# Kernel tuning notes

Hardware: AMD Instinct MI355X
Metric: run time of the kernel (lower is better)

The kernel has to match this reference:

```python
import jax, jax.numpy as jnp
import numpy as np

DN = ('NCHW', 'OIHW', 'NCHW')
A, NC = 3, 80  # num_anchors, num_classes


def conv(x, w, b, pad=1):
    y = jax.lax.conv_general_dilated(x, w, (1, 1), [(pad, pad), (pad, pad)], dimension_numbers=DN)
    return y + b[None, :, None, None]


def up2(x):
    return jnp.repeat(jnp.repeat(x, 2, axis=2), 2, axis=3)


def gen_anchors():
    # AnchorGenerator: sizes per level, 3 aspect ratios, 1 scale, stride=2**(i+3)
    sizes = [32.0, 64.0, 128.0]
    ars = [0.5, 1.0, 2.0]
    hw = [(64, 64), (32, 32), (16, 16)]
    out = []
    for i, ((h, w), bs) in enumerate(zip(hw, sizes)):
        stride = 2.0 ** (i + 3)
        base = np.array([[-bs * np.sqrt(a) / 2, -bs / np.sqrt(a) / 2,
                          bs * np.sqrt(a) / 2, bs / np.sqrt(a) / 2] for a in ars], dtype=np.float32)
        sx = np.arange(w, dtype=np.float32) * stride
        sy = np.arange(h, dtype=np.float32) * stride
        yy, xx = np.meshgrid(sy, sx, indexing='ij')  # torch.meshgrid default 'ij'
        shifts = np.stack([xx.ravel(), yy.ravel(), xx.ravel(), yy.ravel()], axis=1)
        anc = (base[None, :, :] + shifts[:, None, :]).reshape(-1, 4)
        out.append(anc)
    return jnp.asarray(np.concatenate(out, axis=0))


def setup_inputs() -> dict:
    key = jax.random.key(0)
    ks = jax.random.split(key, 32)
    def w(k, o, i, kh, kw):
        return jax.random.normal(k, (o, i, kh, kw), jnp.float32) * 0.02
    B = 8
    inp = {
        'feat3': jax.random.normal(ks[0], (B, 512, 64, 64), jnp.float32),
        'feat4': jax.random.normal(ks[1], (B, 1024, 32, 32), jnp.float32),
        'feat5': jax.random.normal(ks[2], (B, 2048, 16, 16), jnp.float32),
        # FPN lateral 1x1 convs
        'lw0': w(ks[3], 256, 512, 1, 1),  'lb0': jnp.zeros(256, jnp.float32),
        'lw1': w(ks[4], 256, 1024, 1, 1), 'lb1': jnp.zeros(256, jnp.float32),
        'lw2': w(ks[5], 256, 2048, 1, 1), 'lb2': jnp.zeros(256, jnp.float32),
        # FPN 3x3 output convs
        'fw0': w(ks[6], 256, 256, 3, 3), 'fb0': jnp.zeros(256, jnp.float32),
        'fw1': w(ks[7], 256, 256, 3, 3), 'fb1': jnp.zeros(256, jnp.float32),
        'fw2': w(ks[8], 256, 256, 3, 3), 'fb2': jnp.zeros(256, jnp.float32),
        # cls tower (shared across levels)
        'cw0': w(ks[9], 256, 256, 3, 3),  'cb0': jnp.zeros(256, jnp.float32),
        'cw1': w(ks[10], 256, 256, 3, 3), 'cb1': jnp.zeros(256, jnp.float32),
        'cw2': w(ks[11], A * NC, 256, 3, 3), 'cb2': jnp.zeros(A * NC, jnp.float32),
        # reg tower (shared across levels)
        'rw0': w(ks[12], 256, 256, 3, 3), 'rb0': jnp.zeros(256, jnp.float32),
        'rw1': w(ks[13], 256, 256, 3, 3), 'rb1': jnp.zeros(256, jnp.float32),
        'rw2': w(ks[14], A * 4, 256, 3, 3), 'rb2': jnp.zeros(A * 4, jnp.float32),
    }
    return inp


def _tower(f, w0, b0, w1, b1, w2, b2):
    x = jax.nn.relu(conv(f, w0, b0))
    x = jax.nn.relu(conv(x, w1, b1))
    return conv(x, w2, b2)


def reference(feat3, feat4, feat5,
              lw0, lb0, lw1, lb1, lw2, lb2,
              fw0, fb0, fw1, fb1, fw2, fb2,
              cw0, cb0, cw1, cb1, cw2, cb2,
              rw0, rb0, rw1, rb1, rw2, rb2):
    B = feat3.shape[0]
    # FPN: lateral 1x1 convs + top-down nearest upsample fusion + 3x3 convs
    l0 = conv(feat3, lw0, lb0, pad=0)
    l1 = conv(feat4, lw1, lb1, pad=0)
    l2 = conv(feat5, lw2, lb2, pad=0)
    l1 = l1 + up2(l2)
    l0 = l0 + up2(l1)
    feats = [conv(l0, fw0, fb0), conv(l1, fw1, fb1), conv(l2, fw2, fb2)]
    cls_list, reg_list = [], []
    for f in feats:
        c = _tower(f, cw0, cb0, cw1, cb1, cw2, cb2)  # [B, A*NC, H, W]
        r = _tower(f, rw0, rb0, rw1, rb1, rw2, rb2)  # [B, A*4, H, W]
        H, W = c.shape[2], c.shape[3]
        # view(B, A, C, HW).permute(0, 3, 1, 2) -> [B, HW, A, C]
        c = c.reshape(B, A, NC, H * W).transpose(0, 3, 1, 2)
        r = r.reshape(B, A, 4, H * W).transpose(0, 3, 1, 2)
        cls_list.append(c.reshape(B, H * W, A * NC))
        reg_list.append(r.reshape(B, H * W, A * 4))
    cls_all = jnp.concatenate(cls_list, axis=1)   # [B, 5376, 240]
    reg_all = jnp.concatenate(reg_list, axis=1)   # [B, 5376, 12]
    out = jnp.concatenate([cls_all, reg_all], axis=-1)  # [B, 5376, 252]
    anchors = gen_anchors()  # [16128, 4]
    return out, anchors
```

## Files before the change

kernel.cpp:

```cpp
#include <hip/hip_runtime.h>

typedef __bf16 bf16_t;
typedef __bf16 bf16x8 __attribute__((ext_vector_type(8)));
typedef float f32x4 __attribute__((ext_vector_type(4)));

__device__ inline void gl_lds16(const bf16_t* g, bf16_t* l) {
  __builtin_amdgcn_global_load_lds(
      (const __attribute__((address_space(1))) void*)g,
      (__attribute__((address_space(3))) void*)l, 16, 0, 0);
}

__global__ __launch_bounds__(256)
void nchw_to_nhwc(const float* __restrict__ in, bf16_t* __restrict__ out,
                  int C, int HW) {
  __shared__ float tile[64][65];
  const int n = blockIdx.z;
  const int c0 = blockIdx.y * 64, p0 = blockIdx.x * 64;
  const int t = threadIdx.x;
  const float* src = in + ((size_t)n * C + c0) * HW + p0;
  const int cl = t >> 6;
  const int pl = t & 63;
#pragma unroll
  for (int i = 0; i < 16; ++i)
    tile[cl + i * 4][pl] = src[(size_t)(cl + i * 4) * HW + pl];
  __syncthreads();
  bf16_t* dst = out + ((size_t)n * HW + p0) * C + c0;
  const int pc = t >> 6;
  const int cc = t & 63;
#pragma unroll
  for (int i = 0; i < 16; ++i)
    dst[(size_t)(pc + i * 4) * C + cc] = (bf16_t)tile[cc][pc + i * 4];
}

struct WSrc {
  const float *lw0, *lw1, *lw2;
  const float* w9[9];
  int O9[9];
};
__global__ __launch_bounds__(256)
void weight_prep(WSrc s, bf16_t* __restrict__ LWT0, bf16_t* __restrict__ LWT1,
                 bf16_t* __restrict__ LWT2, bf16_t* __restrict__ W33) {
  int idx = blockIdx.x * 256 + threadIdx.x;
  if (idx < 131072) { LWT0[idx] = (bf16_t)s.lw0[idx]; return; }
  if (idx < 393216) { int i = idx - 131072; LWT1[i] = (bf16_t)s.lw1[i]; return; }
  if (idx < 917504) { int i = idx - 393216; LWT2[i] = (bf16_t)s.lw2[i]; return; }
  int t2 = idx - 917504;
  if (t2 >= 9 * 589824) return;
  int sgi = t2 / 589824;
  int r = t2 - sgi * 589824;
  int kid = r >> 16;
  int rem = r & 65535;
  int o = rem >> 8, ci = rem & 255;
  const float* src = s.w9[sgi];
  int O = s.O9[sgi];
  W33[t2] = (o < O) ? (bf16_t)src[((size_t)o * 256 + ci) * 9 + kid] : (bf16_t)0.0f;
}

__global__ __launch_bounds__(256)
void up2_add_p(bf16_t* __restrict__ dst, const bf16_t* __restrict__ src,
               int lw, int lhw, int dWp, int dNs, int sWp, int sNs, int tot8) {
  int idx = blockIdx.x * 256 + threadIdx.x;
  if (idx >= tot8) return;
  const int c8 = idx & 31;
  const int pos = idx >> 5;
  const int n = pos >> lhw;
  const int rem = pos & ((1 << lhw) - 1);
  const int y = rem >> lw, x = rem & ((1 << lw) - 1);
  bf16_t* d = dst + ((size_t)n * dNs + (y + 1) * dWp + (x + 1)) * 256 + c8 * 8;
  const bf16_t* sp = src + ((size_t)n * sNs + ((y >> 1) + 1) * sWp + ((x >> 1) + 1)) * 256 + c8 * 8;
  bf16x8 dv = *(bf16x8*)d;
  bf16x8 sv = *(const bf16x8*)sp;
#pragma unroll
  for (int k = 0; k < 8; ++k) dv[k] = (bf16_t)((float)dv[k] + (float)sv[k]);
  *(bf16x8*)d = dv;
}

struct Job1 {
  const bf16_t* A;
  const bf16_t* Wt;
  const float* bias;
  bf16_t* outb;
  int mtiles, lw, lhw, oWp, onstride, Cin, pad0, pad1;
};
struct Job1Pack { Job1 j[3]; };

__global__ __launch_bounds__(256, 2)
void conv1_batch(Job1Pack jp) {
  __shared__ __align__(16) bf16_t As[128 * 32];
  __shared__ __align__(16) bf16_t Bs[128 * 32];
  int b = blockIdx.x, ji = 0;
#pragma unroll 1
  for (; ji < 2; ++ji) {
    int sz = jp.j[ji].mtiles * 2;
    if (b < sz) break;
    b -= sz;
  }
  const Job1 J = jp.j[ji];
  const int nt = b & 1, mt = b >> 1;
  const int m0 = mt * 128, n0 = nt * 128;
  const int t = threadIdx.x, l = t & 63, w = t >> 6;
  const int W = 1 << J.lw, HW = 1 << J.lhw;
  const int sr = l >> 2, seg = (l & 3) * 8;
  const bf16_t* aptr[2];
  const bf16_t* bptr[2];
  bf16_t* alds[2];
  bf16_t* blds[2];
#pragma unroll
  for (int q = 0; q < 2; ++q) {
    const int r = w * 32 + q * 16 + sr;
    aptr[q] = J.A + (size_t)(m0 + r) * J.Cin + seg;
    alds[q] = &As[(w * 32 + q * 16) * 32];
    bptr[q] = J.Wt + (size_t)(n0 + r) * J.Cin + seg;
    blds[q] = &Bs[(w * 32 + q * 16) * 32];
  }
  const int fr = l & 15, qd = l >> 4;
  const int wm = (w & 1) * 64, wn = (w >> 1) * 64;

  f32x4 acc[4][4];
#pragma unroll
  for (int i = 0; i < 4; ++i)
#pragma unroll
    for (int j = 0; j < 4; ++j)
#pragma unroll
      for (int r = 0; r < 4; ++r) acc[i][j][r] = 0.0f;

  const int kiters = J.Cin >> 5;
#pragma unroll 1
  for (int kk = 0; kk < kiters; ++kk) {
    __syncthreads();
    gl_lds16(aptr[0], alds[0]);
    gl_lds16(aptr[1], alds[1]);
    gl_lds16(bptr[0], blds[0]);
    gl_lds16(bptr[1], blds[1]);
    __syncthreads();
    aptr[0] += 32; aptr[1] += 32; bptr[0] += 32; bptr[1] += 32;
    bf16x8 af[4], bfv[4];
#pragma unroll
    for (int i = 0; i < 4; ++i)
      af[i] = *(const bf16x8*)&As[(wm + i * 16 + fr) * 32 + qd * 8];
#pragma unroll
    for (int j = 0; j < 4; ++j)
      bfv[j] = *(const bf16x8*)&Bs[(wn + j * 16 + fr) * 32 + qd * 8];
#pragma unroll
    for (int i = 0; i < 4; ++i)
#pragma unroll
      for (int j = 0; j < 4; ++j)
        acc[i][j] = __builtin_amdgcn_mfma_f32_16x16x32_bf16(af[i], bfv[j],
                                                            acc[i][j], 0, 0, 0);
  }

#pragma unroll
  for (int i = 0; i < 4; ++i) {
    const int mrow = m0 + wm + i * 16 + qd * 4;
#pragma unroll
    for (int j = 0; j < 4; ++j) {
      const int co = n0 + wn + j * 16 + fr;
      const float bv = J.bias[co];
#pragma unroll
      for (int r = 0; r < 4; ++r) {
        float v = acc[i][j][r] + bv;
        const int m = mrow + r;
        const int n = m >> J.lhw, hw = m & (HW - 1);
        const int y = hw >> J.lw, x = hw & (W - 1);
        J.outb[((size_t)n * J.onstride + (y + 1) * J.oWp + (x + 1)) * 256 + co] =
            (bf16_t)v;
      }
    }
  }
}

struct Job3 {
  const bf16_t* A;
  const bf16_t* Wt;
  const float* bias;
  bf16_t* outb;
  int mtiles, ntiles, lw, lhw, Wp, nsA, oWp, onstride;
  int relu, Cout, pos_off, ch_off, use_outf, nAr, Pc, pad_;
};
struct Job3Pack { Job3 j[6]; };

__global__ __launch_bounds__(256, 3)
void conv3_batch(Job3Pack jp, float* __restrict__ outf) {
  __shared__ __align__(16) bf16_t As[320 * 32];
  __shared__ __align__(16) bf16_t Bs[384 * 32];
  int b = blockIdx.x, ji = 0;
#pragma unroll 1
  for (; ji < 5; ++ji) {
    int sz = jp.j[ji].mtiles * jp.j[ji].ntiles;
    if (b < sz) break;
    b -= sz;
  }
  const Job3 J = jp.j[ji];
  const int nt = (J.ntiles == 2) ? (b & 1) : 0;
  const int mt = (J.ntiles == 2) ? (b >> 1) : b;
  const int m0 = mt * 128, n0 = nt * 128;
  const int t = threadIdx.x, l = t & 63, w = t >> 6;
  const int W = 1 << J.lw, HW = 1 << J.lhw;
  const int sr = l >> 2, seg = (l & 3) * 8;
  const int fr = l & 15, qd = l >> 4;
  const int wm = (w & 1) * 64, wn = (w >> 1) * 64;

  const int n_img = m0 >> J.lhw;
  const int Y0 = (m0 & (HW - 1)) >> J.lw;
  const bf16_t* Ag = J.A + ((size_t)n_img * J.nsA + (size_t)Y0 * J.Wp) * 256;

  int apix[4];
#pragma unroll
  for (int i = 0; i < 4; ++i) {
    const int m = wm + i * 16 + fr;
    const int y = m >> J.lw, x = m & (W - 1);
    apix[i] = ((y + 1) * J.Wp + (x + 1)) * 32 + qd * 8;
  }

  f32x4 acc[4][4];
#pragma unroll
  for (int i = 0; i < 4; ++i)
#pragma unroll
    for (int j = 0; j < 4; ++j)
#pragma unroll
      for (int r = 0; r < 4; ++r) acc[i][j][r] = 0.0f;

#pragma unroll 1
  for (int cb = 0; cb < 8; ++cb) {
    const int cboff = cb * 32;
#pragma unroll 1
    for (int ky = 0; ky < 3; ++ky) {
      __syncthreads();
#pragma unroll
      for (int r = 0; r < 6; ++r) {
        const int R = r * 64 + w * 16 + sr;
        const int tp = R >> 7, co = R & 127;
        gl_lds16(J.Wt + (size_t)(ky * 3 + tp) * 65536 +
                     (size_t)(n0 + co) * 256 + cboff + seg,
                 &Bs[(r * 64 + w * 16) * 32]);
      }
      if (ky == 0) {
#pragma unroll 1
        for (int r = 0; r < J.nAr; ++r) {
          int p = r * 64 + w * 16 + sr;
          p = (p < J.Pc) ? p : (J.Pc - 1);
          gl_lds16(Ag + (size_t)p * 256 + cboff + seg,
                   &As[(r * 64 + w * 16) * 32]);
        }
      }
      __syncthreads();
      const int dyoff = (ky - 1) * J.Wp * 32;
#pragma unroll
      for (int kx = 0; kx < 3; ++kx) {
        const int d = dyoff + (kx - 1) * 32;
        bf16x8 af[4], bfv[4];
#pragma unroll
        for (int i = 0; i < 4; ++i)
          af[i] = *(const bf16x8*)&As[apix[i] + d];
#pragma unroll
        for (int j = 0; j < 4; ++j)
          bfv[j] = *(const bf16x8*)&Bs[(kx * 128 + wn + j * 16 + fr) * 32 + qd * 8];
#pragma unroll
        for (int i = 0; i < 4; ++i)
#pragma unroll
          for (int j = 0; j < 4; ++j)
            acc[i][j] = __builtin_amdgcn_mfma_f32_16x16x32_bf16(af[i], bfv[j],
                                                                acc[i][j], 0, 0, 0);
      }
    }
  }

#pragma unroll
  for (int i = 0; i < 4; ++i) {
    const int mrow = m0 + wm + i * 16 + qd * 4;
#pragma unroll
    for (int j = 0; j < 4; ++j) {
      const int co = n0 + wn + j * 16 + fr;
      if (co < J.Cout) {
        const float bv = J.bias[co];
#pragma unroll
        for (int r = 0; r < 4; ++r) {
          float v = acc[i][j][r] + bv;
          if (J.relu) v = fmaxf(v, 0.0f);
          const int m = mrow + r;
          const int n = m >> J.lhw, hw = m & (HW - 1);
          if (J.use_outf) {
            outf[((size_t)n * 5376 + J.pos_off + hw) * 252 + J.ch_off + co] = v;
          } else {
            const int y = hw >> J.lw, x = hw & (W - 1);
            J.outb[((size_t)n * J.onstride + (y + 1) * J.oWp + (x + 1)) * 256 + co] =
                (bf16_t)v;
          }
        }
      }
    }
  }
}

__global__ __launch_bounds__(256)
void anchors_k(float* __restrict__ out) {
  int r = blockIdx.x * 256 + threadIdx.x;
  if (r >= 16128) return;
  int local, w, stride;
  float bs;
  if (r < 12288)      { local = r;          w = 64; stride = 8;  bs = 32.f;  }
  else if (r < 15360) { local = r - 12288;  w = 32; stride = 16; bs = 64.f;  }
  else                { local = r - 15360;  w = 16; stride = 32; bs = 128.f; }
  const int a = local % 3;
  const int s = local / 3;
  const int y = s / w, x = s - y * w;
  const float ar = (a == 0) ? 0.5f : (a == 1) ? 1.0f : 2.0f;
  const float sq = sqrtf(ar);
  const float hw_ = bs * sq * 0.5f, hh = bs / sq * 0.5f;
  const float cx = (float)x * (float)stride, cy = (float)y * (float)stride;
  out[(size_t)r * 4 + 0] = cx - hw_;
  out[(size_t)r * 4 + 1] = cy - hh;
  out[(size_t)r * 4 + 2] = cx + hw_;
  out[(size_t)r * 4 + 3] = cy + hh;
}

extern "C" void kernel_launch(void* const* d_in, const int* in_sizes, int n_in,
                              void* d_out, int out_size, void* d_ws, size_t ws_size,
                              hipStream_t stream) {
  const float* feat3 = (const float*)d_in[0];
  const float* feat4 = (const float*)d_in[1];
  const float* feat5 = (const float*)d_in[2];
  const float* lw0 = (const float*)d_in[3];  const float* lb0 = (const float*)d_in[4];
  const float* lw1 = (const float*)d_in[5];  const float* lb1 = (const float*)d_in[6];
  const float* lw2 = (const float*)d_in[7];  const float* lb2 = (const float*)d_in[8];
  const float* fw0 = (const float*)d_in[9];  const float* fb0 = (const float*)d_in[10];
  const float* fw1 = (const float*)d_in[11]; const float* fb1 = (const float*)d_in[12];
  const float* fw2 = (const float*)d_in[13]; const float* fb2 = (const float*)d_in[14];
  const float* cw0 = (const float*)d_in[15]; const float* cb0 = (const float*)d_in[16];
  const float* cw1 = (const float*)d_in[17]; const float* cb1 = (const float*)d_in[18];
  const float* cw2 = (const float*)d_in[19]; const float* cb2 = (const float*)d_in[20];
  const float* rw0 = (const float*)d_in[21]; const float* rb0 = (const float*)d_in[22];
  const float* rw1 = (const float*)d_in[23]; const float* rb1 = (const float*)d_in[24];
  const float* rw2 = (const float*)d_in[25]; const float* rb2 = (const float*)d_in[26];

  char* ws = (char*)d_ws;
  float* out = (float*)d_out;

  bf16_t* XS3 = (bf16_t*)(ws + 0);
  bf16_t* XS4 = (bf16_t*)(ws + 33554432);
  bf16_t* XS5 = (bf16_t*)(ws + 50331648);
  bf16_t* Lp0 = (bf16_t*)(ws + 58720256);
  bf16_t* Lp1 = (bf16_t*)(ws + 76562432);
  bf16_t* Lp2 = (bf16_t*)(ws + 81297408);
  bf16_t* Pp0 = (bf16_t*)(ws + 82624512);
  bf16_t* Pp1 = (bf16_t*)(ws + 100466688);
  bf16_t* Pp2 = (bf16_t*)(ws + 105201664);
  bf16_t* LWT0 = (bf16_t*)(ws + 106528768);
  bf16_t* LWT1 = (bf16_t*)(ws + 106790912);
  bf16_t* LWT2 = (bf16_t*)(ws + 107315200);
  bf16_t* W33  = (bf16_t*)(ws + 108363776);
  bf16_t* FWT0 = W33 + 0 * 589824;
  bf16_t* FWT1 = W33 + 1 * 589824;
  bf16_t* FWT2 = W33 + 2 * 589824;
  bf16_t* CWT0 = W33 + 3 * 589824;
  bf16_t* CWT1 = W33 + 4 * 589824;
  bf16_t* CWT2 = W33 + 5 * 589824;
  bf16_t* RWT0 = W33 + 6 * 589824;
  bf16_t* RWT1 = W33 + 7 * 589824;
  bf16_t* RWT2 = W33 + 8 * 589824;
  bf16_t* TAc0 = (bf16_t*)(ws + 0);
  bf16_t* TAr0 = (bf16_t*)(ws + 17842176);
  bf16_t* TAc1 = (bf16_t*)(ws + 35684352);
  bf16_t* TAr1 = (bf16_t*)(ws + 40419328);
  bf16_t* TAc2 = (bf16_t*)(ws + 45154304);
  bf16_t* TAr2 = (bf16_t*)(ws + 46481408);
  bf16_t* TBc0 = Pp0; bf16_t* TBr0 = Lp0;
  bf16_t* TBc1 = Pp1; bf16_t* TBr1 = Lp1;
  bf16_t* TBc2 = Pp2; bf16_t* TBr2 = Lp2;

  WSrc wsrc;
  wsrc.lw0 = lw0; wsrc.lw1 = lw1; wsrc.lw2 = lw2;
  const float* w9s[9] = {fw0, fw1, fw2, cw0, cw1, cw2, rw0, rw1, rw2};
  int o9s[9] = {256, 256, 256, 256, 256, 240, 256, 256, 12};
  for (int i = 0; i < 9; ++i) { wsrc.w9[i] = w9s[i]; wsrc.O9[i] = o9s[i]; }
  weight_prep<<<dim3(24320), 256, 0, stream>>>(wsrc, LWT0, LWT1, LWT2, W33);

  nchw_to_nhwc<<<dim3(64, 8, 8),  256, 0, stream>>>(feat3, XS3, 512, 4096);
  nchw_to_nhwc<<<dim3(16, 16, 8), 256, 0, stream>>>(feat4, XS4, 1024, 1024);
  nchw_to_nhwc<<<dim3(4, 32, 8),  256, 0, stream>>>(feat5, XS5, 2048, 256);

  hipMemsetAsync(ws + 58720256, 0, 47808512, stream);

  {
    Job1Pack jp;
    jp.j[0] = {XS3, LWT0, lb0, Lp0, 256, 6, 12, 66, 4356, 512, 0, 0};
    jp.j[1] = {XS4, LWT1, lb1, Lp1, 64, 5, 10, 34, 1156, 1024, 0, 0};
    jp.j[2] = {XS5, LWT2, lb2, Lp2, 16, 4, 8, 18, 324, 2048, 0, 0};
    conv1_batch<<<dim3(672), 256, 0, stream>>>(jp);
  }

  hipMemsetAsync(ws + 0, 0, 47808512, stream);

  up2_add_p<<<dim3(1024), 256, 0, stream>>>(Lp1, Lp2, 5, 10, 34, 1156, 18, 324, 262144);
  up2_add_p<<<dim3(4096), 256, 0, stream>>>(Lp0, Lp1, 6, 12, 66, 4356, 34, 1156, 1048576);

  auto mk3 = [](const bf16_t* A, const bf16_t* Wt, const float* bias,
                bf16_t* outb, int mtiles, int ntiles, int lw, int lhw,
                int Wp, int nsA, int oWp, int onstride, int relu, int Cout,
                int pos_off, int ch_off, int use_outf, int nAr, int Pc) {
    Job3 j;
    j.A = A; j.Wt = Wt; j.bias = bias; j.outb = outb;
    j.mtiles = mtiles; j.ntiles = ntiles; j.lw = lw; j.lhw = lhw;
    j.Wp = Wp; j.nsA = nsA; j.oWp = oWp; j.onstride = onstride;
    j.relu = relu; j.Cout = Cout; j.pos_off = pos_off; j.ch_off = ch_off;
    j.use_outf = use_outf; j.nAr = nAr; j.Pc = Pc; j.pad_ = 0;
    return j;
  };

  {
    Job3Pack jp;
    jp.j[0] = mk3(Lp0, FWT0, fb0, Pp0, 256, 2, 6, 12, 66, 4356, 66, 4356, 0, 256, 0, 0, 0, 5, 264);
    jp.j[1] = mk3(Lp1, FWT1, fb1, Pp1, 64, 2, 5, 10, 34, 1156, 34, 1156, 0, 256, 0, 0, 0, 4, 204);
    jp.j[2] = mk3(Lp2, FWT2, fb2, Pp2, 16, 2, 4, 8, 18, 324, 18, 324, 0, 256, 0, 0, 0, 3, 180);
    jp.j[3] = jp.j[4] = jp.j[5] = jp.j[2];
    jp.j[3].mtiles = jp.j[4].mtiles = jp.j[5].mtiles = 0;
    conv3_batch<<<dim3(672), 256, 0, stream>>>(jp, out);
  }

  {
    Job3Pack jp;
    jp.j[0] = mk3(Pp0, CWT0, cb0, TAc0, 256, 2, 6, 12, 66, 4356, 66, 4356, 1, 256, 0, 0, 0, 5, 264);
    jp.j[1] = mk3(Pp0, RWT0, rb0, TAr0, 256, 2, 6, 12, 66, 4356, 66, 4356, 1, 256, 0, 0, 0, 5, 264);
    jp.j[2] = mk3(Pp1, CWT0, cb0, TAc1, 64, 2, 5, 10, 34, 1156, 34, 1156, 1, 256, 0, 0, 0, 4, 204);
    jp.j[3] = mk3(Pp1, RWT0, rb0, TAr1, 64, 2, 5, 10, 34, 1156, 34, 1156, 1, 256, 0, 0, 0, 4, 204);
    jp.j[4] = mk3(Pp2, CWT0, cb0, TAc2, 16, 2, 4, 8, 18, 324, 18, 324, 1, 256, 0, 0, 0, 3, 180);
    jp.j[5] = mk3(Pp2, RWT0, rb0, TAr2, 16, 2, 4, 8, 18, 324, 18, 324, 1, 256, 0, 0, 0, 3, 180);
    conv3_batch<<<dim3(1344), 256, 0, stream>>>(jp, out);
  }

  {
    Job3Pack jp;
    jp.j[0] = mk3(TAc0, CWT1, cb1, TBc0, 256, 2, 6, 12, 66, 4356, 66, 4356, 1, 256, 0, 0, 0, 5, 264);
    jp.j[1] = mk3(TAr0, RWT1, rb1, TBr0, 256, 2, 6, 12, 66, 4356, 66, 4356, 1, 256, 0, 0, 0, 5, 264);
    jp.j[2] = mk3(TAc1, CWT1, cb1, TBc1, 64, 2, 5, 10, 34, 1156, 34, 1156, 1, 256, 0, 0, 0, 4, 204);
    jp.j[3] = mk3(TAr1, RWT1, rb1, TBr1, 64, 2, 5, 10, 34, 1156, 34, 1156, 1, 256, 0, 0, 0, 4, 204);
    jp.j[4] = mk3(TAc2, CWT1, cb1, TBc2, 16, 2, 4, 8, 18, 324, 18, 324, 1, 256, 0, 0, 0, 3, 180);
    jp.j[5] = mk3(TAr2, RWT1, rb1, TBr2, 16, 2, 4, 8, 18, 324, 18, 324, 1, 256, 0, 0, 0, 3, 180);
    conv3_batch<<<dim3(1344), 256, 0, stream>>>(jp, out);
  }

  {
    Job3Pack jp;
    jp.j[0] = mk3(TBc0, CWT2, cb2, nullptr, 256, 2, 6, 12, 66, 4356, 0, 0, 0, 240, 0, 0, 1, 5, 264);
    jp.j[1] = mk3(TBr0, RWT2, rb2, nullptr, 256, 1, 6, 12, 66, 4356, 0, 0, 0, 12, 0, 240, 1, 5, 264);
    jp.j[2] = mk3(TBc1, CWT2, cb2, nullptr, 64, 2, 5, 10, 34, 1156, 0, 0, 0, 240, 4096, 0, 1, 4, 204);
    jp.j[3] = mk3(TBr1, RWT2, rb2, nullptr, 64, 1, 5, 10, 34, 1156, 0, 0, 0, 12, 4096, 240, 1, 4, 204);
    jp.j[4] = mk3(TBc2, CWT2, cb2, nullptr, 16, 2, 4, 8, 18, 324, 0, 0, 0, 240, 5120, 0, 1, 3, 180);
    jp.j[5] = mk3(TBr2, RWT2, rb2, nullptr, 16, 1, 4, 8, 18, 324, 0, 0, 0, 12, 5120, 240, 1, 3, 180);
    conv3_batch<<<dim3(1008), 256, 0, stream>>>(jp, out);
  }

  anchors_k<<<dim3(63), 256, 0, stream>>>(out + 10838016);
}
```

Baseline: 664.4 us.

## Double-buffer LDS staging in 1x1 and 3x3 conv GEMM kernels

```diff
diff --git a/kernel.cpp b/kernel.cpp
--- a/kernel.cpp
+++ b/kernel.cpp
@@ -86,8 +86,8 @@
 
 __global__ __launch_bounds__(256, 2)
 void conv1_batch(Job1Pack jp) {
-  __shared__ __align__(16) bf16_t As[128 * 32];
-  __shared__ __align__(16) bf16_t Bs[128 * 32];
+  __shared__ __align__(16) bf16_t As[2][128 * 32];
+  __shared__ __align__(16) bf16_t Bs[2][128 * 32];
   int b = blockIdx.x, ji = 0;
 #pragma unroll 1
   for (; ji < 2; ++ji) {
@@ -103,15 +103,13 @@
   const int sr = l >> 2, seg = (l & 3) * 8;
   const bf16_t* aptr[2];
   const bf16_t* bptr[2];
-  bf16_t* alds[2];
-  bf16_t* blds[2];
+  int lrow[2];
 #pragma unroll
   for (int q = 0; q < 2; ++q) {
     const int r = w * 32 + q * 16 + sr;
     aptr[q] = J.A + (size_t)(m0 + r) * J.Cin + seg;
-    alds[q] = &As[(w * 32 + q * 16) * 32];
     bptr[q] = J.Wt + (size_t)(n0 + r) * J.Cin + seg;
-    blds[q] = &Bs[(w * 32 + q * 16) * 32];
+    lrow[q] = (w * 32 + q * 16) * 32;
   }
   const int fr = l & 15, qd = l >> 4;
   const int wm = (w & 1) * 64, wn = (w >> 1) * 64;
@@ -123,24 +121,30 @@
     for (int j = 0; j < 4; ++j)
 #pragma unroll
       for (int r = 0; r < 4; ++r) acc[i][j][r] = 0.0f;
+
+  auto stage = [&](int buf, int kk) {
+#pragma unroll
+    for (int q = 0; q < 2; ++q) {
+      gl_lds16(aptr[q] + (size_t)kk * 32, &As[buf][lrow[q]]);
+      gl_lds16(bptr[q] + (size_t)kk * 32, &Bs[buf][lrow[q]]);
+    }
+  };
+
+  stage(0, 0);
 
   const int kiters = J.Cin >> 5;
 #pragma unroll 1
   for (int kk = 0; kk < kiters; ++kk) {
+    const int cur = kk & 1;
     __syncthreads();
-    gl_lds16(aptr[0], alds[0]);
-    gl_lds16(aptr[1], alds[1]);
-    gl_lds16(bptr[0], blds[0]);
-    gl_lds16(bptr[1], blds[1]);
-    __syncthreads();
-    aptr[0] += 32; aptr[1] += 32; bptr[0] += 32; bptr[1] += 32;
+    if (kk + 1 < kiters) stage(cur ^ 1, kk + 1);
     bf16x8 af[4], bfv[4];
 #pragma unroll
     for (int i = 0; i < 4; ++i)
-      af[i] = *(const bf16x8*)&As[(wm + i * 16 + fr) * 32 + qd * 8];
+      af[i] = *(const bf16x8*)&As[cur][(wm + i * 16 + fr) * 32 + qd * 8];
 #pragma unroll
     for (int j = 0; j < 4; ++j)
-      bfv[j] = *(const bf16x8*)&Bs[(wn + j * 16 + fr) * 32 + qd * 8];
+      bfv[j] = *(const bf16x8*)&Bs[cur][(wn + j * 16 + fr) * 32 + qd * 8];
 #pragma unroll
     for (int i = 0; i < 4; ++i)
 #pragma unroll
@@ -179,10 +183,10 @@
 };
 struct Job3Pack { Job3 j[6]; };
 
-__global__ __launch_bounds__(256, 3)
+__global__ __launch_bounds__(256, 2)
 void conv3_batch(Job3Pack jp, float* __restrict__ outf) {
   __shared__ __align__(16) bf16_t As[320 * 32];
-  __shared__ __align__(16) bf16_t Bs[384 * 32];
+  __shared__ __align__(16) bf16_t Bs[2][384 * 32];
   int b = blockIdx.x, ji = 0;
 #pragma unroll 1
   for (; ji < 5; ++ji) {
@@ -199,6 +203,7 @@
   const int sr = l >> 2, seg = (l & 3) * 8;
   const int fr = l & 15, qd = l >> 4;
   const int wm = (w & 1) * 64, wn = (w >> 1) * 64;
+  const int wrow = w * 16 + sr;
 
   const int n_img = m0 >> J.lhw;
   const int Y0 = (m0 & (HW - 1)) >> J.lw;
@@ -220,49 +225,67 @@
 #pragma unroll
       for (int r = 0; r < 4; ++r) acc[i][j][r] = 0.0f;
 
+  auto stageB = [&](int buf, int ky, int cboff) {
+#pragma unroll
+    for (int r = 0; r < 6; ++r) {
+      const int R = r * 64 + wrow;
+      const int tp = R >> 7, co = R & 127;
+      gl_lds16(J.Wt + (size_t)(ky * 3 + tp) * 65536 +
+                   (size_t)(n0 + co) * 256 + cboff + seg,
+               &Bs[buf][(r * 64 + w * 16) * 32]);
+    }
+  };
+  auto stageA = [&](int cboff) {
 #pragma unroll 1
-  for (int cb = 0; cb < 8; ++cb) {
-    const int cboff = cb * 32;
+    for (int r = 0; r < J.nAr; ++r) {
+      int p = r * 64 + wrow;
+      p = (p < J.Pc) ? p : (J.Pc - 1);
+      gl_lds16(Ag + (size_t)p * 256 + cboff + seg,
+               &As[(r * 64 + w * 16) * 32]);
+    }
+  };
+
+  stageA(0);
+  stageB(0, 0, 0);
+
+  int cb = 0, ky = 0;
 #pragma unroll 1
-    for (int ky = 0; ky < 3; ++ky) {
-      __syncthreads();
-#pragma unroll
-      for (int r = 0; r < 6; ++r) {
-        const int R = r * 64 + w * 16 + sr;
-        const int tp = R >> 7, co = R & 127;
-        gl_lds16(J.Wt + (size_t)(ky * 3 + tp) * 65536 +
-                     (size_t)(n0 + co) * 256 + cboff + seg,
-                 &Bs[(r * 64 + w * 16) * 32]);
+  for (int p = 0; p < 24; ++p) {
+    const int cur = p & 1;
+    __syncthreads();
+    if (p < 23) {
+      int kyn = ky + 1, cbn = cb;
+      if (kyn == 3) { kyn = 0; cbn = cb + 1; }
+      stageB(cur ^ 1, kyn, cbn * 32);
+    }
+    const bool aB = (ky == 2) && (cb < 7);
+    const int dyoff = (ky - 1) * J.Wp * 32;
+#pragma unroll
+    for (int kx = 0; kx < 3; ++kx) {
+      const int d = dyoff + (kx - 1) * 32;
+      bf16x8 af[4], bfv[4];
+#pragma unroll
+      for (int i = 0; i < 4; ++i)
+        af[i] = *(const bf16x8*)&As[apix[i] + d];
+#pragma unroll
+      for (int j = 0; j < 4; ++j)
+        bfv[j] = *(const bf16x8*)&Bs[cur][(kx * 128 + wn + j * 16 + fr) * 32 + qd * 8];
+      if (kx == 2 && aB) {
+        asm volatile("s_waitcnt lgkmcnt(0)" ::: "memory");
+        __builtin_amdgcn_sched_barrier(0);
+        __builtin_amdgcn_s_barrier();
+        __builtin_amdgcn_sched_barrier(0);
+        stageA((cb + 1) * 32);
       }
-      if (ky == 0) {
-#pragma unroll 1
-        for (int r = 0; r < J.nAr; ++r) {
-          int p = r * 64 + w * 16 + sr;
-          p = (p < J.Pc) ? p : (J.Pc - 1);
-          gl_lds16(Ag + (size_t)p * 256 + cboff + seg,
-                   &As[(r * 64 + w * 16) * 32]);
-        }
-      }
-      __syncthreads();
-      const int dyoff = (ky - 1) * J.Wp * 32;
-#pragma unroll
-      for (int kx = 0; kx < 3; ++kx) {
-        const int d = dyoff + (kx - 1) * 32;
-        bf16x8 af[4], bfv[4];
-#pragma unroll
-        for (int i = 0; i < 4; ++i)
-          af[i] = *(const bf16x8*)&As[apix[i] + d];
+#pragma unroll
+      for (int i = 0; i < 4; ++i)
 #pragma unroll
         for (int j = 0; j < 4; ++j)
-          bfv[j] = *(const bf16x8*)&Bs[(kx * 128 + wn + j * 16 + fr) * 32 + qd * 8];
-#pragma unroll
-        for (int i = 0; i < 4; ++i)
-#pragma unroll
-          for (int j = 0; j < 4; ++j)
-            acc[i][j] = __builtin_amdgcn_mfma_f32_16x16x32_bf16(af[i], bfv[j],
-                                                                acc[i][j], 0, 0, 0);
-      }
-    }
+          acc[i][j] = __builtin_amdgcn_mfma_f32_16x16x32_bf16(af[i], bfv[j],
+                                                              acc[i][j], 0, 0, 0);
+    }
+    ky = (ky == 2) ? 0 : ky + 1;
+    if (ky == 0) ++cb;
   }
 
 #pragma unroll
```

New measurement: 723.4 us. +8.9%, slower.

## Double-buffer 1x1 conv LDS, swizzle block order, group cls/reg tower jobs

Applied to the files above, without the earlier changes.

```diff
diff --git a/kernel.cpp b/kernel.cpp
--- a/kernel.cpp
+++ b/kernel.cpp
@@ -86,9 +86,11 @@
 
 __global__ __launch_bounds__(256, 2)
 void conv1_batch(Job1Pack jp) {
-  __shared__ __align__(16) bf16_t As[128 * 32];
-  __shared__ __align__(16) bf16_t Bs[128 * 32];
-  int b = blockIdx.x, ji = 0;
+  __shared__ __align__(16) bf16_t As[2][128 * 32];
+  __shared__ __align__(16) bf16_t Bs[2][128 * 32];
+  const int cpx = gridDim.x >> 3;
+  int b = (blockIdx.x & 7) * cpx + (blockIdx.x >> 3);
+  int ji = 0;
 #pragma unroll 1
   for (; ji < 2; ++ji) {
     int sz = jp.j[ji].mtiles * 2;
@@ -103,15 +105,13 @@
   const int sr = l >> 2, seg = (l & 3) * 8;
   const bf16_t* aptr[2];
   const bf16_t* bptr[2];
-  bf16_t* alds[2];
-  bf16_t* blds[2];
+  int lrow[2];
 #pragma unroll
   for (int q = 0; q < 2; ++q) {
     const int r = w * 32 + q * 16 + sr;
     aptr[q] = J.A + (size_t)(m0 + r) * J.Cin + seg;
-    alds[q] = &As[(w * 32 + q * 16) * 32];
     bptr[q] = J.Wt + (size_t)(n0 + r) * J.Cin + seg;
-    blds[q] = &Bs[(w * 32 + q * 16) * 32];
+    lrow[q] = (w * 32 + q * 16) * 32;
   }
   const int fr = l & 15, qd = l >> 4;
   const int wm = (w & 1) * 64, wn = (w >> 1) * 64;
@@ -124,23 +124,29 @@
 #pragma unroll
       for (int r = 0; r < 4; ++r) acc[i][j][r] = 0.0f;
 
+  auto stage = [&](int buf, int kk) {
+#pragma unroll
+    for (int q = 0; q < 2; ++q) {
+      gl_lds16(aptr[q] + (size_t)kk * 32, &As[buf][lrow[q]]);
+      gl_lds16(bptr[q] + (size_t)kk * 32, &Bs[buf][lrow[q]]);
+    }
+  };
+
+  stage(0, 0);
+
   const int kiters = J.Cin >> 5;
 #pragma unroll 1
   for (int kk = 0; kk < kiters; ++kk) {
+    const int cur = kk & 1;
     __syncthreads();
-    gl_lds16(aptr[0], alds[0]);
-    gl_lds16(aptr[1], alds[1]);
-    gl_lds16(bptr[0], blds[0]);
-    gl_lds16(bptr[1], blds[1]);
-    __syncthreads();
-    aptr[0] += 32; aptr[1] += 32; bptr[0] += 32; bptr[1] += 32;
+    if (kk + 1 < kiters) stage(cur ^ 1, kk + 1);
     bf16x8 af[4], bfv[4];
 #pragma unroll
     for (int i = 0; i < 4; ++i)
-      af[i] = *(const bf16x8*)&As[(wm + i * 16 + fr) * 32 + qd * 8];
+      af[i] = *(const bf16x8*)&As[cur][(wm + i * 16 + fr) * 32 + qd * 8];
 #pragma unroll
     for (int j = 0; j < 4; ++j)
-      bfv[j] = *(const bf16x8*)&Bs[(wn + j * 16 + fr) * 32 + qd * 8];
+      bfv[j] = *(const bf16x8*)&Bs[cur][(wn + j * 16 + fr) * 32 + qd * 8];
 #pragma unroll
     for (int i = 0; i < 4; ++i)
 #pragma unroll
@@ -174,6 +180,9 @@
   const bf16_t* Wt;
   const float* bias;
   bf16_t* outb;
+  const bf16_t* Wt2;
+  const float* bias2;
+  bf16_t* outb2;
   int mtiles, ntiles, lw, lhw, Wp, nsA, oWp, onstride;
   int relu, Cout, pos_off, ch_off, use_outf, nAr, Pc, pad_;
 };
@@ -183,7 +192,9 @@
 void conv3_batch(Job3Pack jp, float* __restrict__ outf) {
   __shared__ __align__(16) bf16_t As[320 * 32];
   __shared__ __align__(16) bf16_t Bs[384 * 32];
-  int b = blockIdx.x, ji = 0;
+  const int cpx = gridDim.x >> 3;
+  int b = (blockIdx.x & 7) * cpx + (blockIdx.x >> 3);
+  int ji = 0;
 #pragma unroll 1
   for (; ji < 5; ++ji) {
     int sz = jp.j[ji].mtiles * jp.j[ji].ntiles;
@@ -191,9 +202,16 @@
     b -= sz;
   }
   const Job3 J = jp.j[ji];
-  const int nt = (J.ntiles == 2) ? (b & 1) : 0;
-  const int mt = (J.ntiles == 2) ? (b >> 1) : b;
-  const int m0 = mt * 128, n0 = nt * 128;
+  int s, mt;
+  if (J.ntiles == 4)      { s = b & 3; mt = b >> 2; }
+  else if (J.ntiles == 2) { s = b & 1; mt = b >> 1; }
+  else                    { s = 0;     mt = b; }
+  const int second = (s >= 2);
+  const int n0 = (s & 1) * 128;
+  const bf16_t* Wtp = second ? J.Wt2 : J.Wt;
+  const float* biasp = second ? J.bias2 : J.bias;
+  bf16_t* outbp = second ? J.outb2 : J.outb;
+  const int m0 = mt * 128;
   const int t = threadIdx.x, l = t & 63, w = t >> 6;
   const int W = 1 << J.lw, HW = 1 << J.lhw;
   const int sr = l >> 2, seg = (l & 3) * 8;
@@ -230,7 +248,7 @@
       for (int r = 0; r < 6; ++r) {
         const int R = r * 64 + w * 16 + sr;
         const int tp = R >> 7, co = R & 127;
-        gl_lds16(J.Wt + (size_t)(ky * 3 + tp) * 65536 +
+        gl_lds16(Wtp + (size_t)(ky * 3 + tp) * 65536 +
                      (size_t)(n0 + co) * 256 + cboff + seg,
                  &Bs[(r * 64 + w * 16) * 32]);
       }
@@ -272,7 +290,7 @@
     for (int j = 0; j < 4; ++j) {
       const int co = n0 + wn + j * 16 + fr;
       if (co < J.Cout) {
-        const float bv = J.bias[co];
+        const float bv = biasp[co];
 #pragma unroll
         for (int r = 0; r < 4; ++r) {
           float v = acc[i][j][r] + bv;
@@ -283,7 +301,7 @@
             outf[((size_t)n * 5376 + J.pos_off + hw) * 252 + J.ch_off + co] = v;
           } else {
             const int y = hw >> J.lw, x = hw & (W - 1);
-            J.outb[((size_t)n * J.onstride + (y + 1) * J.oWp + (x + 1)) * 256 + co] =
+            outbp[((size_t)n * J.onstride + (y + 1) * J.oWp + (x + 1)) * 256 + co] =
                 (bf16_t)v;
           }
         }
@@ -400,6 +418,7 @@
                 int pos_off, int ch_off, int use_outf, int nAr, int Pc) {
     Job3 j;
     j.A = A; j.Wt = Wt; j.bias = bias; j.outb = outb;
+    j.Wt2 = Wt; j.bias2 = bias; j.outb2 = outb;
     j.mtiles = mtiles; j.ntiles = ntiles; j.lw = lw; j.lhw = lhw;
     j.Wp = Wp; j.nsA = nsA; j.oWp = oWp; j.onstride = onstride;
     j.relu = relu; j.Cout = Cout; j.pos_off = pos_off; j.ch_off = ch_off;
@@ -419,12 +438,14 @@
 
   {
     Job3Pack jp;
-    jp.j[0] = mk3(Pp0, CWT0, cb0, TAc0, 256, 2, 6, 12, 66, 4356, 66, 4356, 1, 256, 0, 0, 0, 5, 264);
-    jp.j[1] = mk3(Pp0, RWT0, rb0, TAr0, 256, 2, 6, 12, 66, 4356, 66, 4356, 1, 256, 0, 0, 0, 5, 264);
-    jp.j[2] = mk3(Pp1, CWT0, cb0, TAc1, 64, 2, 5, 10, 34, 1156, 34, 1156, 1, 256, 0, 0, 0, 4, 204);
-    jp.j[3] = mk3(Pp1, RWT0, rb0, TAr1, 64, 2, 5, 10, 34, 1156, 34, 1156, 1, 256, 0, 0, 0, 4, 204);
-    jp.j[4] = mk3(Pp2, CWT0, cb0, TAc2, 16, 2, 4, 8, 18, 324, 18, 324, 1, 256, 0, 0, 0, 3, 180);
-    jp.j[5] = mk3(Pp2, RWT0, rb0, TAr2, 16, 2, 4, 8, 18, 324, 18, 324, 1, 256, 0, 0, 0, 3, 180);
+    jp.j[0] = mk3(Pp0, CWT0, cb0, TAc0, 256, 4, 6, 12, 66, 4356, 66, 4356, 1, 256, 0, 0, 0, 5, 264);
+    jp.j[0].Wt2 = RWT0; jp.j[0].bias2 = rb0; jp.j[0].outb2 = TAr0;
+    jp.j[1] = mk3(Pp1, CWT0, cb0, TAc1, 64, 4, 5, 10, 34, 1156, 34, 1156, 1, 256, 0, 0, 0, 4, 204);
+    jp.j[1].Wt2 = RWT0; jp.j[1].bias2 = rb0; jp.j[1].outb2 = TAr1;
+    jp.j[2] = mk3(Pp2, CWT0, cb0, TAc2, 16, 4, 4, 8, 18, 324, 18, 324, 1, 256, 0, 0, 0, 3, 180);
+    jp.j[2].Wt2 = RWT0; jp.j[2].bias2 = rb0; jp.j[2].outb2 = TAr2;
+    jp.j[3] = jp.j[4] = jp.j[5] = jp.j[2];
+    jp.j[3].mtiles = jp.j[4].mtiles = jp.j[5].mtiles = 0;
     conv3_batch<<<dim3(1344), 256, 0, stream>>>(jp, out);
   }
 
```

Measured after the change: 674.1 us. No clear change (+1.5%).
